# Performance work log

Measured on AMD Instinct MI355X. Metric: run time of the kernel, lower is better.

The kernel has to match this reference:

```python
import jax, jax.numpy as jnp
import numpy as np

B, T, D = 16, 2048, 256

def setup_inputs() -> dict:
    key = jax.random.key(0)
    k1, k2, k3 = jax.random.split(key, 3)
    q = jax.random.normal(k1, (B, T, D), dtype=jnp.float32)
    a = jax.random.normal(k2, (B, T, D), dtype=jnp.float32)
    # original uses 'uniform' init; scale ~ small
    U = jax.random.uniform(k3, (D, D), dtype=jnp.float32, minval=-0.05, maxval=0.05)
    return {"q": q, "a": a, "U": U}

def reference(q, a, U):
    # G[b,i,j] = tanh( (q[b,i,:] @ U) . a[b,j,:] )
    qU = jnp.einsum('btd,de->bte', q, U)                 # [B,Tq,D]
    G = jnp.tanh(jnp.einsum('btd,bsd->bts', qU, a))      # [B,Tq,Ta]
    g_q = jax.nn.softmax(jnp.max(G, axis=-1), axis=1)    # [B,Tq]
    g_a = jax.nn.softmax(jnp.max(G, axis=1), axis=1)     # [B,Ta]
    q_out = jnp.einsum('btd,bt->bd', q, g_q)             # [B,D]
    a_out = jnp.einsum('bsd,bs->bd', a, g_a)             # [B,D]
    return (q_out, a_out)
```

## Files before the change

### kernel.cpp

```cpp
#include <hip/hip_runtime.h>
#include <stdint.h>

typedef __attribute__((ext_vector_type(8))) short s8v;
typedef __attribute__((ext_vector_type(4))) float f4v;

__device__ __forceinline__ unsigned short f2bf(float f) {
  unsigned u = __float_as_uint(f);
  u = u + 0x7FFFu + ((u >> 16) & 1u);
  return (unsigned short)(u >> 16);
}
__device__ __forceinline__ unsigned encf(float f) {
  unsigned i = __float_as_uint(f);
  return (i & 0x80000000u) ? ~i : (i | 0x80000000u);
}
__device__ __forceinline__ float decf(unsigned u) {
  unsigned i = (u & 0x80000000u) ? (u & 0x7FFFFFFFu) : ~u;
  return __uint_as_float(i);
}
__device__ __forceinline__ void gload_lds16(const unsigned short* g, unsigned short* l) {
  __builtin_amdgcn_global_load_lds((const __attribute__((address_space(1))) void*)g,
                                   (__attribute__((address_space(3))) void*)l, 16, 0, 0);
}

__global__ void convert_kernel(const float4* __restrict__ q, const float4* __restrict__ a,
                               const float* __restrict__ U,
                               ushort4* __restrict__ qb, ushort4* __restrict__ ab,
                               unsigned short* __restrict__ Ut,
                               unsigned* __restrict__ rcmax) {
  const int bx = blockIdx.x;
  if (bx < 8192) {
    const int i = bx * 256 + threadIdx.x;
    float4 v = q[i];
    qb[i] = make_ushort4(f2bf(v.x), f2bf(v.y), f2bf(v.z), f2bf(v.w));
    float4 w = a[i];
    ab[i] = make_ushort4(f2bf(w.x), f2bf(w.y), f2bf(w.z), f2bf(w.w));
  } else if (bx < 8256) {
    const int idx = (bx - 8192) * 256 + threadIdx.x;
    const int n  = idx >> 6;
    const int k4 = (idx & 63) * 4;
    ushort4 o;
    o.x = f2bf(U[(k4 + 0) * 256 + n]);
    o.y = f2bf(U[(k4 + 1) * 256 + n]);
    o.z = f2bf(U[(k4 + 2) * 256 + n]);
    o.w = f2bf(U[(k4 + 3) * 256 + n]);
    *(ushort4*)&Ut[n * 256 + k4] = o;
  } else {
    const int idx = (bx - 8256) * 256 + threadIdx.x;
    *(uint4*)&rcmax[idx * 4] = make_uint4(0u, 0u, 0u, 0u);
  }
}

template<int MODE>
__global__ void gemm_bt(const unsigned short* __restrict__ A,
                        const unsigned short* __restrict__ Bm,
                        long strideA, long strideB,
                        unsigned short* __restrict__ C,
                        unsigned* __restrict__ rowmax,
                        unsigned* __restrict__ colmax,
                        float* __restrict__ outz) {
  constexpr int AROWS = 128;
  constexpr int BROWS = 128;
  constexpr int RPI = 32;

  __shared__ unsigned short As[AROWS * 64];
  __shared__ unsigned short Bs[BROWS * 64];
  __shared__ unsigned rowLds[AROWS];
  __shared__ unsigned colLds[BROWS];

  const int tid = threadIdx.x;
  int tm, tn, b;
  if (MODE == 1) { b = blockIdx.x; tn = blockIdx.y; tm = blockIdx.z; }
  else           { tm = blockIdx.x; tn = blockIdx.y; b = blockIdx.z; }
  const unsigned short* Ab = A + (long)b * strideA + (long)tm * AROWS * 256;
  const unsigned short* Bb = Bm + (long)b * strideB + (long)tn * BROWS * 256;

  const int lane = tid & 63;
  const int m16  = lane & 15;
  const int quad = lane >> 4;
  const int wave = tid >> 6;
  const int wm   = wave >> 1, wn = wave & 1;
  const int srow = tid >> 3;
  const int scol = (((tid & 7) ^ (srow & 7))) * 8;

  if (MODE == 1) {
    if (tid < AROWS) rowLds[tid] = 0u;
    if (tid < BROWS) colLds[tid] = 0u;
    if (tn == 0 && tm == 0) {
      outz[b * 256 + tid] = 0.f;
      outz[4096 + b * 256 + tid] = 0.f;
    }
  }

  f4v acc[4][4] = {};

  for (int kt = 0; kt < 4; ++kt) {
    const int k0 = kt * 64;
    __syncthreads();
    #pragma unroll
    for (int i = 0; i < AROWS / RPI; ++i) {
      const int r = i * RPI + srow;
      gload_lds16(Ab + (long)r * 256 + k0 + scol, &As[i * RPI * 64 + tid * 8]);
    }
    #pragma unroll
    for (int i = 0; i < BROWS / RPI; ++i) {
      const int r = i * RPI + srow;
      gload_lds16(Bb + (long)r * 256 + k0 + scol, &Bs[i * RPI * 64 + tid * 8]);
    }
    __syncthreads();
    #pragma unroll
    for (int kk = 0; kk < 2; ++kk) {
      const int cs = ((kk * 4 + quad) ^ (m16 & 7)) * 8;
      s8v af[4], bfv[4];
      #pragma unroll
      for (int i = 0; i < 4; ++i)
        af[i] = *(const s8v*)&As[(wm * 64 + i * 16 + m16) * 64 + cs];
      #pragma unroll
      for (int j = 0; j < 4; ++j)
        bfv[j] = *(const s8v*)&Bs[(wn * 64 + j * 16 + m16) * 64 + cs];
      #pragma unroll
      for (int i = 0; i < 4; ++i)
        #pragma unroll
        for (int j = 0; j < 4; ++j)
          acc[i][j] = __builtin_amdgcn_mfma_f32_16x16x32_bf16(af[i], bfv[j], acc[i][j], 0, 0, 0);
    }
  }

  if (MODE == 0) {
    #pragma unroll
    for (int i = 0; i < 4; ++i)
      #pragma unroll
      for (int r = 0; r < 4; ++r) {
        const long row = (long)tm * AROWS + wm * 64 + i * 16 + quad * 4 + r;
        #pragma unroll
        for (int j = 0; j < 4; ++j) {
          const int col = tn * BROWS + wn * 64 + j * 16 + m16;
          C[row * 256 + col] = f2bf(acc[i][j][r]);
        }
      }
  } else {
    #pragma unroll
    for (int i = 0; i < 4; ++i)
      #pragma unroll
      for (int r = 0; r < 4; ++r) {
        float v = fmaxf(fmaxf(acc[i][0][r], acc[i][1][r]), fmaxf(acc[i][2][r], acc[i][3][r]));
        #pragma unroll
        for (int d2 = 1; d2 < 16; d2 <<= 1) v = fmaxf(v, __shfl_xor(v, d2));
        if (m16 == 0) atomicMax(&rowLds[wm * 64 + i * 16 + quad * 4 + r], encf(v));
      }
    #pragma unroll
    for (int j = 0; j < 4; ++j) {
      float v = -3.4e38f;
      #pragma unroll
      for (int i = 0; i < 4; ++i)
        #pragma unroll
        for (int r = 0; r < 4; ++r) v = fmaxf(v, acc[i][j][r]);
      v = fmaxf(v, __shfl_xor(v, 16));
      v = fmaxf(v, __shfl_xor(v, 32));
      if (quad == 0) atomicMax(&colLds[wn * 64 + j * 16 + m16], encf(v));
    }
    __syncthreads();
    if (tid < AROWS) {
      atomicMax(&rowmax[(long)b * 2048 + tm * AROWS + tid], rowLds[tid]);
    } else if (tid < AROWS + BROWS) {
      atomicMax(&colmax[(long)b * 2048 + tn * BROWS + (tid - AROWS)], colLds[tid - AROWS]);
    }
  }
}

__global__ void wsum_kernel(const uint4* __restrict__ qb, const uint4* __restrict__ ab,
                            const unsigned* __restrict__ rowmax, const unsigned* __restrict__ colmax,
                            float* __restrict__ out) {
  const int tid = threadIdx.x;
  const int chunk = blockIdx.x;
  const int b = blockIdx.y;
  const int z = blockIdx.z;
  const unsigned* e = z ? colmax : rowmax;
  const uint4* src = z ? ab : qb;

  __shared__ float sm[4];
  __shared__ float ss[4];
  __shared__ float wLds[128];
  __shared__ float red[256 * 8];

  float x[8];
  float m = -3.4e38f;
  #pragma unroll
  for (int j = 0; j < 8; ++j) {
    x[j] = tanhf(decf(e[b * 2048 + j * 256 + tid]));
    m = fmaxf(m, x[j]);
  }
  #pragma unroll
  for (int d2 = 1; d2 < 64; d2 <<= 1) m = fmaxf(m, __shfl_xor(m, d2));
  if ((tid & 63) == 0) sm[tid >> 6] = m;
  __syncthreads();
  m = fmaxf(fmaxf(sm[0], sm[1]), fmaxf(sm[2], sm[3]));
  float s = 0.f;
  #pragma unroll
  for (int j = 0; j < 8; ++j) s += expf(x[j] - m);
  #pragma unroll
  for (int d2 = 1; d2 < 64; d2 <<= 1) s += __shfl_xor(s, d2);
  if ((tid & 63) == 0) ss[tid >> 6] = s;
  __syncthreads();
  const float inv = 1.f / (ss[0] + ss[1] + ss[2] + ss[3]);

  if (tid < 128) {
    float xv = tanhf(decf(e[b * 2048 + chunk * 128 + tid]));
    wLds[tid] = expf(xv - m) * inv;
  }
  __syncthreads();

  const int dg = tid & 31;
  const int rg = tid >> 5;
  float acc[8] = {};
  const long rowbase = (long)b * 2048 + chunk * 128;
  for (int t = rg; t < 128; t += 8) {
    const float wgt = wLds[t];
    uint4 v = src[(rowbase + t) * 32 + dg];
    acc[0] += wgt * __uint_as_float(v.x << 16);
    acc[1] += wgt * __uint_as_float(v.x & 0xFFFF0000u);
    acc[2] += wgt * __uint_as_float(v.y << 16);
    acc[3] += wgt * __uint_as_float(v.y & 0xFFFF0000u);
    acc[4] += wgt * __uint_as_float(v.z << 16);
    acc[5] += wgt * __uint_as_float(v.z & 0xFFFF0000u);
    acc[6] += wgt * __uint_as_float(v.w << 16);
    acc[7] += wgt * __uint_as_float(v.w & 0xFFFF0000u);
  }
  #pragma unroll
  for (int k = 0; k < 8; ++k) red[tid * 8 + k] = acc[k];
  __syncthreads();
  if (tid < 32) {
    #pragma unroll
    for (int k = 0; k < 8; ++k) {
      float v = 0.f;
      #pragma unroll
      for (int g = 0; g < 8; ++g) v += red[((g << 5) | tid) * 8 + k];
      atomicAdd(&out[z * 4096 + b * 256 + tid * 8 + k], v);
    }
  }
}

extern "C" void kernel_launch(void* const* d_in, const int* in_sizes, int n_in,
                              void* d_out, int out_size, void* d_ws, size_t ws_size,
                              hipStream_t stream) {
  const float* q = (const float*)d_in[0];
  const float* a = (const float*)d_in[1];
  const float* U = (const float*)d_in[2];
  float* out = (float*)d_out;

  char* w = (char*)d_ws;
  unsigned short* qb = (unsigned short*)w;
  unsigned short* ab = (unsigned short*)(w + (16ull << 20));
  unsigned short* qU = (unsigned short*)(w + (32ull << 20));
  unsigned short* Ut = (unsigned short*)(w + (48ull << 20));
  unsigned* rmax = (unsigned*)(w + (48ull << 20) + (128ull << 10));
  unsigned* cmax = rmax + 32768;

  convert_kernel<<<8192 + 64 + 64, 256, 0, stream>>>((const float4*)q, (const float4*)a, U,
                                                     (ushort4*)qb, (ushort4*)ab, Ut, rmax);

  gemm_bt<0><<<dim3(256, 2, 1), 256, 0, stream>>>(qb, Ut, 0, 0, qU,
                                                  nullptr, nullptr, nullptr);

  gemm_bt<1><<<dim3(16, 16, 16), 256, 0, stream>>>(qU, ab, 2048 * 256, 2048 * 256,
                                                   nullptr, rmax, cmax, out);

  wsum_kernel<<<dim3(16, 16, 2), 256, 0, stream>>>((const uint4*)qb, (const uint4*)ab,
                                                   rmax, cmax, out);
}
```

Baseline: 178.6 us.

## Fuse q·U projection into score-max kernel with LDS-resident qU tile

```diff
diff --git a/kernel.cpp b/kernel.cpp
--- a/kernel.cpp
+++ b/kernel.cpp
@@ -26,7 +26,7 @@
                                const float* __restrict__ U,
                                ushort4* __restrict__ qb, ushort4* __restrict__ ab,
                                unsigned short* __restrict__ Ut,
-                               unsigned* __restrict__ rcmax) {
+                               unsigned* __restrict__ rcmax, float* __restrict__ out) {
   const int bx = blockIdx.x;
   if (bx < 8192) {
     const int i = bx * 256 + threadIdx.x;
@@ -44,35 +44,28 @@
     o.z = f2bf(U[(k4 + 2) * 256 + n]);
     o.w = f2bf(U[(k4 + 3) * 256 + n]);
     *(ushort4*)&Ut[n * 256 + k4] = o;
-  } else {
+  } else if (bx < 8320) {
     const int idx = (bx - 8256) * 256 + threadIdx.x;
     *(uint4*)&rcmax[idx * 4] = make_uint4(0u, 0u, 0u, 0u);
-  }
-}
-
-template<int MODE>
-__global__ void gemm_bt(const unsigned short* __restrict__ A,
-                        const unsigned short* __restrict__ Bm,
-                        long strideA, long strideB,
-                        unsigned short* __restrict__ C,
-                        unsigned* __restrict__ rowmax,
-                        unsigned* __restrict__ colmax,
-                        float* __restrict__ outz) {
-  constexpr int AROWS = 128;
-  constexpr int BROWS = 128;
-  constexpr int RPI = 32;
-
-  __shared__ unsigned short As[AROWS * 64];
-  __shared__ unsigned short Bs[BROWS * 64];
-  __shared__ unsigned rowLds[AROWS];
-  __shared__ unsigned colLds[BROWS];
+  } else {
+    out[(bx - 8320) * 256 + threadIdx.x] = 0.f;
+  }
+}
+
+__global__ __launch_bounds__(256, 2)
+void fused_qu_smax(const unsigned short* __restrict__ qb,
+                   const unsigned short* __restrict__ Ut,
+                   const unsigned short* __restrict__ ab,
+                   unsigned* __restrict__ rowmax,
+                   unsigned* __restrict__ colmax) {
+  extern __shared__ char smem[];
+  unsigned short* qUs   = (unsigned short*)smem;
+  unsigned short* Bs2   = (unsigned short*)(smem + 65536);
+  unsigned*       colLds = (unsigned*)(smem + 131072);
+  unsigned*       rowLds = (unsigned*)(smem + 139264);
 
   const int tid = threadIdx.x;
-  int tm, tn, b;
-  if (MODE == 1) { b = blockIdx.x; tn = blockIdx.y; tm = blockIdx.z; }
-  else           { tm = blockIdx.x; tn = blockIdx.y; b = blockIdx.z; }
-  const unsigned short* Ab = A + (long)b * strideA + (long)tm * AROWS * 256;
-  const unsigned short* Bb = Bm + (long)b * strideB + (long)tn * BROWS * 256;
+  const int b = blockIdx.x, tm = blockIdx.y;
 
   const int lane = tid & 63;
   const int m16  = lane & 15;
@@ -82,70 +75,99 @@
   const int srow = tid >> 3;
   const int scol = (((tid & 7) ^ (srow & 7))) * 8;
 
-  if (MODE == 1) {
-    if (tid < AROWS) rowLds[tid] = 0u;
-    if (tid < BROWS) colLds[tid] = 0u;
-    if (tn == 0 && tm == 0) {
-      outz[b * 256 + tid] = 0.f;
-      outz[4096 + b * 256 + tid] = 0.f;
-    }
-  }
-
-  f4v acc[4][4] = {};
-
-  for (int kt = 0; kt < 4; ++kt) {
-    const int k0 = kt * 64;
+  #pragma unroll
+  for (int i = 0; i < 8; ++i) colLds[i * 256 + tid] = 0u;
+  if (tid < 128) rowLds[tid] = 0u;
+
+  const unsigned short* Aq = qb + ((long)b * 2048 + tm * 128) * 256;
+  unsigned short* S1 = Bs2;
+  unsigned short* S2 = Bs2 + 8192;
+  #pragma unroll 1
+  for (int nh = 0; nh < 2; ++nh) {
+    f4v acc[4][4] = {};
+    const unsigned short* Bu = Ut + nh * 128 * 256;
+    for (int kt = 0; kt < 4; ++kt) {
+      const int k0 = kt * 64;
+      __syncthreads();
+      #pragma unroll
+      for (int i = 0; i < 4; ++i)
+        gload_lds16(Aq + (long)(i * 32 + srow) * 256 + k0 + scol, &S1[i * 2048 + tid * 8]);
+      #pragma unroll
+      for (int i = 0; i < 4; ++i)
+        gload_lds16(Bu + (long)(i * 32 + srow) * 256 + k0 + scol, &S2[i * 2048 + tid * 8]);
+      __syncthreads();
+      #pragma unroll
+      for (int kk = 0; kk < 2; ++kk) {
+        const int cs = ((kk * 4 + quad) ^ (m16 & 7)) * 8;
+        s8v af[4], bfv[4];
+        #pragma unroll
+        for (int i = 0; i < 4; ++i)
+          af[i] = *(const s8v*)&S1[(wm * 64 + i * 16 + m16) * 64 + cs];
+        #pragma unroll
+        for (int j = 0; j < 4; ++j)
+          bfv[j] = *(const s8v*)&S2[(wn * 64 + j * 16 + m16) * 64 + cs];
+        #pragma unroll
+        for (int i = 0; i < 4; ++i)
+          #pragma unroll
+          for (int j = 0; j < 4; ++j)
+            acc[i][j] = __builtin_amdgcn_mfma_f32_16x16x32_bf16(af[i], bfv[j], acc[i][j], 0, 0, 0);
+      }
+    }
+    #pragma unroll
+    for (int i = 0; i < 4; ++i)
+      #pragma unroll
+      for (int r = 0; r < 4; ++r) {
+        const int lr = wm * 64 + i * 16 + quad * 4 + r;
+        #pragma unroll
+        for (int j = 0; j < 4; ++j) {
+          const int col = nh * 128 + wn * 64 + j * 16 + m16;
+          const int ch = (col >> 3) ^ (lr & 7);
+          qUs[lr * 256 + ch * 8 + (col & 7)] = f2bf(acc[i][j][r]);
+        }
+      }
+  }
+  __syncthreads();
+
+  const unsigned short* Ab_ = ab + (long)b * 2048 * 256;
+  float rmx[4][4];
+  #pragma unroll
+  for (int i = 0; i < 4; ++i)
+    #pragma unroll
+    for (int r = 0; r < 4; ++r) rmx[i][r] = -3.4e38f;
+
+  #pragma unroll 1
+  for (int tb = 0; tb < 16; ++tb) {
+    #pragma unroll
+    for (int e = 0; e < 16; ++e) {
+      const int u = e * 256 + tid;
+      const int row = u >> 5;
+      const int chs = (u & 31) ^ (row & 7);
+      gload_lds16(Ab_ + (long)(tb * 128 + row) * 256 + chs * 8, &Bs2[u * 8]);
+    }
     __syncthreads();
-    #pragma unroll
-    for (int i = 0; i < AROWS / RPI; ++i) {
-      const int r = i * RPI + srow;
-      gload_lds16(Ab + (long)r * 256 + k0 + scol, &As[i * RPI * 64 + tid * 8]);
-    }
-    #pragma unroll
-    for (int i = 0; i < BROWS / RPI; ++i) {
-      const int r = i * RPI + srow;
-      gload_lds16(Bb + (long)r * 256 + k0 + scol, &Bs[i * RPI * 64 + tid * 8]);
-    }
-    __syncthreads();
-    #pragma unroll
-    for (int kk = 0; kk < 2; ++kk) {
-      const int cs = ((kk * 4 + quad) ^ (m16 & 7)) * 8;
+    f4v acc[4][4] = {};
+    #pragma unroll
+    for (int kq = 0; kq < 8; ++kq) {
+      const int cs = ((kq * 4 + quad) ^ (m16 & 7)) * 8;
       s8v af[4], bfv[4];
       #pragma unroll
       for (int i = 0; i < 4; ++i)
-        af[i] = *(const s8v*)&As[(wm * 64 + i * 16 + m16) * 64 + cs];
+        af[i] = *(const s8v*)&qUs[(wm * 64 + i * 16 + m16) * 256 + cs];
       #pragma unroll
       for (int j = 0; j < 4; ++j)
-        bfv[j] = *(const s8v*)&Bs[(wn * 64 + j * 16 + m16) * 64 + cs];
+        bfv[j] = *(const s8v*)&Bs2[(wn * 64 + j * 16 + m16) * 256 + cs];
       #pragma unroll
       for (int i = 0; i < 4; ++i)
         #pragma unroll
         for (int j = 0; j < 4; ++j)
           acc[i][j] = __builtin_amdgcn_mfma_f32_16x16x32_bf16(af[i], bfv[j], acc[i][j], 0, 0, 0);
     }
-  }
-
-  if (MODE == 0) {
-    #pragma unroll
-    for (int i = 0; i < 4; ++i)
-      #pragma unroll
-      for (int r = 0; r < 4; ++r) {
-        const long row = (long)tm * AROWS + wm * 64 + i * 16 + quad * 4 + r;
-        #pragma unroll
-        for (int j = 0; j < 4; ++j) {
-          const int col = tn * BROWS + wn * 64 + j * 16 + m16;
-          C[row * 256 + col] = f2bf(acc[i][j][r]);
-        }
-      }
-  } else {
     #pragma unroll
     for (int i = 0; i < 4; ++i)
       #pragma unroll
       for (int r = 0; r < 4; ++r) {
         float v = fmaxf(fmaxf(acc[i][0][r], acc[i][1][r]), fmaxf(acc[i][2][r], acc[i][3][r]));
-        #pragma unroll
-        for (int d2 = 1; d2 < 16; d2 <<= 1) v = fmaxf(v, __shfl_xor(v, d2));
-        if (m16 == 0) atomicMax(&rowLds[wm * 64 + i * 16 + quad * 4 + r], encf(v));
+        rmx[i][r] = fmaxf(rmx[i][r], v);
       }
     #pragma unroll
     for (int j = 0; j < 4; ++j) {
@@ -156,15 +178,26 @@
         for (int r = 0; r < 4; ++r) v = fmaxf(v, acc[i][j][r]);
       v = fmaxf(v, __shfl_xor(v, 16));
       v = fmaxf(v, __shfl_xor(v, 32));
-      if (quad == 0) atomicMax(&colLds[wn * 64 + j * 16 + m16], encf(v));
+      if (quad == 0) atomicMax(&colLds[tb * 128 + wn * 64 + j * 16 + m16], encf(v));
     }
     __syncthreads();
-    if (tid < AROWS) {
-      atomicMax(&rowmax[(long)b * 2048 + tm * AROWS + tid], rowLds[tid]);
-    } else if (tid < AROWS + BROWS) {
-      atomicMax(&colmax[(long)b * 2048 + tn * BROWS + (tid - AROWS)], colLds[tid - AROWS]);
-    }
-  }
+  }
+
+  #pragma unroll
+  for (int i = 0; i < 4; ++i)
+    #pragma unroll
+    for (int r = 0; r < 4; ++r) {
+      float v = rmx[i][r];
+      #pragma unroll
+      for (int d2 = 1; d2 < 16; d2 <<= 1) v = fmaxf(v, __shfl_xor(v, d2));
+      if (m16 == 0) atomicMax(&rowLds[wm * 64 + i * 16 + quad * 4 + r], encf(v));
+    }
+  __syncthreads();
+  if (tid < 128)
+    rowmax[(long)b * 2048 + tm * 128 + tid] = rowLds[tid];
+  #pragma unroll
+  for (int i = 0; i < 8; ++i)
+    atomicMax(&colmax[(long)b * 2048 + i * 256 + tid], colLds[i * 256 + tid]);
 }
 
 __global__ void wsum_kernel(const uint4* __restrict__ qb, const uint4* __restrict__ ab,
@@ -250,19 +283,18 @@
   char* w = (char*)d_ws;
   unsigned short* qb = (unsigned short*)w;
   unsigned short* ab = (unsigned short*)(w + (16ull << 20));
-  unsigned short* qU = (unsigned short*)(w + (32ull << 20));
-  unsigned short* Ut = (unsigned short*)(w + (48ull << 20));
-  unsigned* rmax = (unsigned*)(w + (48ull << 20) + (128ull << 10));
+  unsigned short* Ut = (unsigned short*)(w + (32ull << 20));
+  unsigned* rmax = (unsigned*)(w + (32ull << 20) + (128ull << 10));
   unsigned* cmax = rmax + 32768;
 
-  convert_kernel<<<8192 + 64 + 64, 256, 0, stream>>>((const float4*)q, (const float4*)a, U,
-                                                     (ushort4*)qb, (ushort4*)ab, Ut, rmax);
-
-  gemm_bt<0><<<dim3(256, 2, 1), 256, 0, stream>>>(qb, Ut, 0, 0, qU,
-                                                  nullptr, nullptr, nullptr);
-
-  gemm_bt<1><<<dim3(16, 16, 16), 256, 0, stream>>>(qU, ab, 2048 * 256, 2048 * 256,
-                                                   nullptr, rmax, cmax, out);
+  constexpr int SMEM = 139776;
+  hipFuncSetAttribute((const void*)fused_qu_smax,
+                      hipFuncAttributeMaxDynamicSharedMemorySize, SMEM);
+
+  convert_kernel<<<8352, 256, 0, stream>>>((const float4*)q, (const float4*)a, U,
+                                           (ushort4*)qb, (ushort4*)ab, Ut, rmax, out);
+
+  fused_qu_smax<<<dim3(16, 16), 256, SMEM, stream>>>(qb, Ut, ab, rmax, cmax);
 
   wsum_kernel<<<dim3(16, 16, 2), 256, 0, stream>>>((const uint4*)qb, (const uint4*)ab,
                                                    rmax, cmax, out);
```

Result: faster. 171.9 us (-3.8%).
